# Kernel optimization log

Measured on AMD Instinct MI355X. Metric: run time of the kernel, lower is better.

The kernel has to match this reference:

```python
import jax, jax.numpy as jnp
import numpy as np

N = 4096  # rows == cols so the original's range(len(d1)) loop covers the full tensor
EPS = 1e-05


def setup_inputs() -> dict:
    key = jax.random.key(0)
    k1, k2 = jax.random.split(key)
    distribution1 = jax.random.uniform(k1, (N, N), dtype=jnp.float32)
    distribution2 = jax.random.uniform(k2, (N, N), dtype=jnp.float32)
    return {"distribution1": distribution1, "distribution2": distribution2}


def reference(distribution1, distribution2):
    d1 = jnp.squeeze(distribution1).astype(jnp.float32)
    d2 = jnp.squeeze(distribution2).astype(jnp.float32)
    # loss = sum_i [ -sum_j d1[i,j] * log(d2[i,j] + eps) ]  (fused elementwise + full reduce)
    loss = -jnp.sum(d1 * jnp.log(d2 + EPS))
    return loss.reshape(1)
```

## Files before the change

kernel.cpp:

```cpp
#include <hip/hip_runtime.h>
#include <math.h>


#define EPS 1e-5f

__global__ void cep_zero_kernel(float* out) {
    out[0] = 0.0f;
}

__global__ __launch_bounds__(256) void cep_loss_kernel(
        const float4* __restrict__ d1,
        const float4* __restrict__ d2,
        float* __restrict__ out,
        int n4) {
    int tid = blockIdx.x * blockDim.x + threadIdx.x;
    int stride = gridDim.x * blockDim.x;

    float acc = 0.0f;
    for (int i = tid; i < n4; i += stride) {
        float4 a = d1[i];
        float4 b = d2[i];
        acc += a.x * __logf(b.x + EPS);
        acc += a.y * __logf(b.y + EPS);
        acc += a.z * __logf(b.z + EPS);
        acc += a.w * __logf(b.w + EPS);
    }

    #pragma unroll
    for (int off = 32; off > 0; off >>= 1)
        acc += __shfl_down(acc, off, 64);

    __shared__ float wave_sums[4];
    int lane = threadIdx.x & 63;
    int wid  = threadIdx.x >> 6;
    if (lane == 0) wave_sums[wid] = acc;
    __syncthreads();

    if (threadIdx.x == 0) {
        float s = wave_sums[0] + wave_sums[1] + wave_sums[2] + wave_sums[3];
        atomicAdd(out, -s);
    }
}

extern "C" void kernel_launch(void* const* d_in, const int* in_sizes, int n_in,
                              void* d_out, int out_size, void* d_ws, size_t ws_size,
                              hipStream_t stream) {
    const float4* d1 = (const float4*)d_in[0];
    const float4* d2 = (const float4*)d_in[1];
    float* out = (float*)d_out;

    int n = in_sizes[0];
    int n4 = n / 4;

    cep_zero_kernel<<<1, 1, 0, stream>>>(out);

    const int block = 256;
    const int grid = 2048;
    cep_loss_kernel<<<grid, block, 0, stream>>>(d1, d2, out, n4);
}
```

Measured before the change: 155.4 us.

## Issue all loads up front via inline asm and use two-pass partial reduction

```diff
diff --git a/kernel.cpp b/kernel.cpp
--- a/kernel.cpp
+++ b/kernel.cpp
@@ -3,34 +3,66 @@
 
 
 #define EPS 1e-5f
+#define BLOCK 256
 
-__global__ void cep_zero_kernel(float* out) {
-    out[0] = 0.0f;
-}
+typedef float v4f __attribute__((ext_vector_type(4)));
 
-__global__ __launch_bounds__(256) void cep_loss_kernel(
-        const float4* __restrict__ d1,
-        const float4* __restrict__ d2,
-        float* __restrict__ out,
-        int n4) {
-    int tid = blockIdx.x * blockDim.x + threadIdx.x;
-    int stride = gridDim.x * blockDim.x;
+__global__ __launch_bounds__(BLOCK) void cep_loss_kernel(
+        const float* __restrict__ d1,
+        const float* __restrict__ d2,
+        float* __restrict__ partials) {
+    size_t t = (size_t)blockIdx.x * BLOCK + threadIdx.x;
+    const char* p1 = (const char*)d1 + t * 64;
+    const char* p2 = (const char*)d2 + t * 64;
 
-    float acc = 0.0f;
-    for (int i = tid; i < n4; i += stride) {
-        float4 a = d1[i];
-        float4 b = d2[i];
-        acc += a.x * __logf(b.x + EPS);
-        acc += a.y * __logf(b.y + EPS);
-        acc += a.z * __logf(b.z + EPS);
-        acc += a.w * __logf(b.w + EPS);
-    }
+    v4f a0, b0, a1, b1, a2, b2, a3, b3;
+    asm volatile(
+        "global_load_dwordx4 %0, %8, off\n\t"
+        "global_load_dwordx4 %1, %9, off\n\t"
+        "global_load_dwordx4 %2, %8, off offset:16\n\t"
+        "global_load_dwordx4 %3, %9, off offset:16\n\t"
+        "global_load_dwordx4 %4, %8, off offset:32\n\t"
+        "global_load_dwordx4 %5, %9, off offset:32\n\t"
+        "global_load_dwordx4 %6, %8, off offset:48\n\t"
+        "global_load_dwordx4 %7, %9, off offset:48\n\t"
+        : "=v"(a0), "=v"(b0), "=v"(a1), "=v"(b1),
+          "=v"(a2), "=v"(b2), "=v"(a3), "=v"(b3)
+        : "v"(p1), "v"(p2)
+        : "memory");
+
+    float acc0, acc1, acc2, acc3;
+
+    asm volatile("s_waitcnt vmcnt(6)" : "+v"(a0), "+v"(b0));
+    acc0 = a0.x * __logf(b0.x + EPS);
+    acc1 = a0.y * __logf(b0.y + EPS);
+    acc2 = a0.z * __logf(b0.z + EPS);
+    acc3 = a0.w * __logf(b0.w + EPS);
+
+    asm volatile("s_waitcnt vmcnt(4)" : "+v"(a1), "+v"(b1));
+    acc0 += a1.x * __logf(b1.x + EPS);
+    acc1 += a1.y * __logf(b1.y + EPS);
+    acc2 += a1.z * __logf(b1.z + EPS);
+    acc3 += a1.w * __logf(b1.w + EPS);
+
+    asm volatile("s_waitcnt vmcnt(2)" : "+v"(a2), "+v"(b2));
+    acc0 += a2.x * __logf(b2.x + EPS);
+    acc1 += a2.y * __logf(b2.y + EPS);
+    acc2 += a2.z * __logf(b2.z + EPS);
+    acc3 += a2.w * __logf(b2.w + EPS);
+
+    asm volatile("s_waitcnt vmcnt(0)" : "+v"(a3), "+v"(b3));
+    acc0 += a3.x * __logf(b3.x + EPS);
+    acc1 += a3.y * __logf(b3.y + EPS);
+    acc2 += a3.z * __logf(b3.z + EPS);
+    acc3 += a3.w * __logf(b3.w + EPS);
+
+    float acc = (acc0 + acc1) + (acc2 + acc3);
 
     #pragma unroll
     for (int off = 32; off > 0; off >>= 1)
         acc += __shfl_down(acc, off, 64);
 
-    __shared__ float wave_sums[4];
+    __shared__ float wave_sums[BLOCK / 64];
     int lane = threadIdx.x & 63;
     int wid  = threadIdx.x >> 6;
     if (lane == 0) wave_sums[wid] = acc;
@@ -38,23 +70,43 @@
 
     if (threadIdx.x == 0) {
         float s = wave_sums[0] + wave_sums[1] + wave_sums[2] + wave_sums[3];
-        atomicAdd(out, -s);
+        partials[blockIdx.x] = s;
+    }
+}
+
+__global__ __launch_bounds__(BLOCK) void cep_final_kernel(
+        const float* __restrict__ partials, float* __restrict__ out, int nparts) {
+    float acc = 0.0f;
+    for (int i = threadIdx.x; i < nparts; i += BLOCK)
+        acc += partials[i];
+
+    #pragma unroll
+    for (int off = 32; off > 0; off >>= 1)
+        acc += __shfl_down(acc, off, 64);
+
+    __shared__ float wave_sums[BLOCK / 64];
+    int lane = threadIdx.x & 63;
+    int wid  = threadIdx.x >> 6;
+    if (lane == 0) wave_sums[wid] = acc;
+    __syncthreads();
+
+    if (threadIdx.x == 0) {
+        float s = wave_sums[0] + wave_sums[1] + wave_sums[2] + wave_sums[3];
+        out[0] = -s;
     }
 }
 
 extern "C" void kernel_launch(void* const* d_in, const int* in_sizes, int n_in,
                               void* d_out, int out_size, void* d_ws, size_t ws_size,
                               hipStream_t stream) {
-    const float4* d1 = (const float4*)d_in[0];
-    const float4* d2 = (const float4*)d_in[1];
+    const float* d1 = (const float*)d_in[0];
+    const float* d2 = (const float*)d_in[1];
     float* out = (float*)d_out;
+    float* partials = (float*)d_ws;
 
     int n = in_sizes[0];
-    int n4 = n / 4;
+    const int grid = n / (BLOCK * 16);
 
-    cep_zero_kernel<<<1, 1, 0, stream>>>(out);
-
-    const int block = 256;
-    const int grid = 2048;
-    cep_loss_kernel<<<grid, block, 0, stream>>>(d1, d2, out, n4);
+    cep_loss_kernel<<<grid, BLOCK, 0, stream>>>(d1, d2, partials);
+    cep_final_kernel<<<1, BLOCK, 0, stream>>>(partials, out, grid);
 }
```

Measured after the change: 145.0 us. -6.7%, faster.
